# Performance work log

Measured on AMD Instinct MI355X. Metric: run time of the kernel, lower is better.

Reference implementation:

```python
import jax, jax.numpy as jnp
import numpy as np

N = 20000      # nodes per side
E = 160000     # edges
C = 512        # input_channels
C_OUT = 512    # output_channels
TEMP = float(np.sqrt(C))  # self.temperature = sqrt(input_channels)
NEG_SLOPE = 0.01          # LeakyReLU default


def _xavier(key, shape):
    fan_in, fan_out = shape[1], shape[0]
    std = np.sqrt(2.0 / (fan_in + fan_out))
    return jax.random.normal(key, shape, dtype=jnp.float32) * std


def setup_inputs() -> dict:
    key = jax.random.key(0)
    ks = jax.random.split(key, 10)
    return {
        "node_left": jax.random.normal(ks[0], (N, C), dtype=jnp.float32),
        "segmentation_index_left": jax.random.randint(ks[1], (E,), 0, N),
        "index_left": jax.random.randint(ks[2], (E,), 0, N),
        "node_right": jax.random.normal(ks[3], (N, C), dtype=jnp.float32),
        "segmentation_index_right": jax.random.randint(ks[4], (E,), 0, N),
        "index_right": jax.random.randint(ks[5], (E,), 0, N),
        "Wk": _xavier(ks[6], (C, C)),      # key_projection.weight
        "Wv": _xavier(ks[7], (C, C)),      # value_projection.weight
        "Wo": _xavier(ks[8], (C_OUT, C)),  # out_projection Linear weight
        "bo": jnp.zeros((C_OUT,), dtype=jnp.float32),
    }


def segment_softmax(scores, seg_idx, num_segments, temperature):
    # numerically stable softmax over variable-length segments of edges
    s = scores / temperature
    m = jax.ops.segment_max(s, seg_idx, num_segments=num_segments)
    m = jnp.where(jnp.isneginf(m), 0.0, m)  # guard empty segments
    e = jnp.exp(s - m[seg_idx])
    z = jax.ops.segment_sum(e, seg_idx, num_segments=num_segments)
    return e / z[seg_idx]


def _message(translation, seg_idx, num_segments, neighbor, Wo, bo):
    attn = segment_softmax(translation, seg_idx, num_segments, TEMP)  # [E]
    # dropout is identity at inference
    msg = jax.ops.segment_sum(attn[:, None] * neighbor, seg_idx,
                              num_segments=num_segments)  # [N, C]
    h = msg @ Wo.T + bo
    return jnp.where(h >= 0, h, NEG_SLOPE * h)  # LeakyReLU


def reference(node_left, segmentation_index_left, index_left,
              node_right, segmentation_index_right, index_right,
              Wk, Wv, Wo, bo):
    n_left = node_left.shape[0]
    n_right = node_right.shape[0]
    # key projections gathered to edges
    left_center = (node_left @ Wk.T)[segmentation_index_left]    # [E, C]
    right_center = (node_right @ Wk.T)[segmentation_index_right]  # [E, C]
    # value projections gathered to edges (cross side)
    left_neighbor = (node_right @ Wv.T)[segmentation_index_right]  # [E, C]
    right_neighbor = (node_left @ Wv.T)[segmentation_index_left]   # [E, C]
    translation = jnp.sum(left_center * right_center, axis=1)      # [E]
    msg_left = _message(translation, segmentation_index_left, n_left,
                        left_neighbor, Wo, bo)
    msg_right = _message(translation, segmentation_index_right, n_right,
                         right_neighbor, Wo, bo)
    return (msg_left, msg_right)
```

## Files before the change

kernel.cpp:

```cpp
#include <hip/hip_runtime.h>


#define C_DIM 512
#define TEMP_INV (1.0f / 22.627416997969522f)

using bf16x8 = __attribute__((ext_vector_type(8))) __bf16;
using s16x8  = __attribute__((ext_vector_type(8))) short;
using s16x4  = __attribute__((ext_vector_type(4))) short;
using f32x4  = __attribute__((ext_vector_type(4))) float;

__device__ __forceinline__ float bf2f(short u) {
    union { unsigned u; float f; } t;
    t.u = ((unsigned)(unsigned short)u) << 16;
    return t.f;
}
__device__ __forceinline__ short f2bf(float f) {
    union { float f; unsigned u; } t;
    t.f = f;
    unsigned r = t.u + 0x7FFFu + ((t.u >> 16) & 1u);
    return (short)(r >> 16);
}

__global__ void cvt2_f32_bf16(const float* __restrict__ inA,
                              const float* __restrict__ inB,
                              short* __restrict__ out, long n4half) {
    long i = (long)blockIdx.x * blockDim.x + threadIdx.x;
    long stride = (long)gridDim.x * blockDim.x;
    long n4 = 2 * n4half;
    for (; i < n4; i += stride) {
        const float4* src = (i < n4half)
            ? reinterpret_cast<const float4*>(inA) + i
            : reinterpret_cast<const float4*>(inB) + (i - n4half);
        float4 v = *src;
        s16x4 o;
        o[0] = f2bf(v.x); o[1] = f2bf(v.y); o[2] = f2bf(v.z); o[3] = f2bf(v.w);
        reinterpret_cast<s16x4*>(out)[i] = o;
    }
}

__global__ void cvt_weights(const float* __restrict__ Wk,
                            const float* __restrict__ Wv,
                            const float* __restrict__ Wo,
                            short* __restrict__ WkT, short* __restrict__ WvT,
                            short* __restrict__ WoB) {
    int b = blockIdx.x;
    int tid = threadIdx.x;
    if (b < 128) {
        const float* src = (b < 64) ? Wv : Wk;
        short* dst = (b < 64) ? WvT : WkT;
        int bb = b & 63;
        __shared__ float t[64][65];
        int bx = bb & 7, by = bb >> 3;
#pragma unroll
        for (int i = 0; i < 4; ++i) {
            int idx = i * 256 + tid;
            int row = idx >> 4, c4 = idx & 15;
            float4 v = *(const float4*)&src[(size_t)(by * 64 + row) * 512 + bx * 64 + c4 * 4];
            t[row][c4 * 4 + 0] = v.x; t[row][c4 * 4 + 1] = v.y;
            t[row][c4 * 4 + 2] = v.z; t[row][c4 * 4 + 3] = v.w;
        }
        __syncthreads();
#pragma unroll
        for (int i = 0; i < 4; ++i) {
            int idx = i * 256 + tid;
            int row = idx >> 4, g = idx & 15;
            s16x4 o;
            o[0] = f2bf(t[g * 4 + 0][row]);
            o[1] = f2bf(t[g * 4 + 1][row]);
            o[2] = f2bf(t[g * 4 + 2][row]);
            o[3] = f2bf(t[g * 4 + 3][row]);
            *(s16x4*)&dst[(size_t)(bx * 64 + row) * 512 + by * 64 + g * 4] = o;
        }
    } else {
        long base = (long)(b & 63) * 1024;
#pragma unroll
        for (int i = 0; i < 4; ++i) {
            long idx = base + i * 256 + tid;
            float4 v = reinterpret_cast<const float4*>(Wo)[idx];
            s16x4 o;
            o[0] = f2bf(v.x); o[1] = f2bf(v.y); o[2] = f2bf(v.z); o[3] = f2bf(v.w);
            reinterpret_cast<s16x4*>(WoB)[idx] = o;
        }
    }
}

__global__ __launch_bounds__(256, 4)
void gemm_dual(const short* __restrict__ A0, const short* __restrict__ B0,
               short* __restrict__ C0, int M0, int t0,
               const short* __restrict__ A1, const short* __restrict__ B1,
               short* __restrict__ C1, int M1, int total) {
    __shared__ short As[2][128 * 32];
    __shared__ short Bs[2][128 * 32];

    const int bid = blockIdx.x;
    const int q = total >> 3, r = total & 7;
    const int xcd = bid & 7, idx = bid >> 3;
    const int swz = (xcd < r ? xcd * (q + 1) : r * (q + 1) + (xcd - r) * q) + idx;

    const short* A; const short* B; short* Cp; int M; int tile;
    if (swz < t0) { A = A0; B = B0; Cp = C0; M = M0; tile = swz; }
    else          { A = A1; B = B1; Cp = C1; M = M1; tile = swz - t0; }
    const int bm = (tile >> 2) * 128;
    const int bn = (tile & 3) * 128;
    const int K = C_DIM;

    const int tid  = threadIdx.x;
    const int lane = tid & 63;
    const int wid  = tid >> 6;
    const int wm   = (wid >> 1) * 64;
    const int wn   = (wid & 1) * 64;
    const int lrow  = lane & 15;
    const int khalf = lane >> 4;

    auto stage = [&](short* dA, short* dB, int k0) {
#pragma unroll
        for (int j = 0; j < 2; ++j) {
            int L    = j * 256 + tid;
            int pr   = L >> 3;
            int slot = L & 7;
            int g    = slot ^ (pr & 7);
            int row  = pr * 2 + (g >> 2);
            int kg   = g & 3;
            int wb   = (j * 256 + (tid & ~63)) * 16;
            {
                int grow = bm + row; if (grow >= M) grow = M - 1;
                const short* src = A + (size_t)grow * K + k0 + kg * 8;
                __builtin_amdgcn_global_load_lds(
                    (__attribute__((address_space(1))) void*)src,
                    (__attribute__((address_space(3))) void*)((char*)dA + wb),
                    16, 0, 0);
            }
            {
                int grow = bn + row;
                const short* src = B + (size_t)grow * K + k0 + kg * 8;
                __builtin_amdgcn_global_load_lds(
                    (__attribute__((address_space(1))) void*)src,
                    (__attribute__((address_space(3))) void*)((char*)dB + wb),
                    16, 0, 0);
            }
        }
    };

    auto frag = [&](const short* h, int row) -> bf16x8 {
        int pr   = row >> 1;
        int g    = ((row & 1) << 2) | khalf;
        int slot = g ^ (pr & 7);
        return *(const bf16x8*)&h[pr * 64 + slot * 8];
    };

    f32x4 acc[4][4] = {};
    const int nt = K >> 5;

    stage(As[0], Bs[0], 0);

    for (int t = 0; t < nt; ++t) {
        const int cur = t & 1;
        if (t + 1 < nt) {
            stage(As[cur ^ 1], Bs[cur ^ 1], (t + 1) << 5);
            asm volatile("s_waitcnt vmcnt(4)" ::: "memory");
        } else {
            asm volatile("s_waitcnt vmcnt(0)" ::: "memory");
        }
        __builtin_amdgcn_s_barrier();

        const short* as = As[cur];
        const short* bs = Bs[cur];
        bf16x8 af[4], bfr[4];
#pragma unroll
        for (int m = 0; m < 4; ++m) af[m] = frag(as, wm + m * 16 + lrow);
#pragma unroll
        for (int n = 0; n < 4; ++n) bfr[n] = frag(bs, wn + n * 16 + lrow);

        asm volatile("s_waitcnt lgkmcnt(0)" ::: "memory");
        __builtin_amdgcn_sched_barrier(0);
        __builtin_amdgcn_s_barrier();

        __builtin_amdgcn_s_setprio(1);
#pragma unroll
        for (int m = 0; m < 4; ++m)
#pragma unroll
            for (int n = 0; n < 4; ++n)
                acc[m][n] = __builtin_amdgcn_mfma_f32_16x16x32_bf16(
                    af[m], bfr[n], acc[m][n], 0, 0, 0);
        __builtin_amdgcn_s_setprio(0);
    }

    const int crow0 = (lane >> 4) * 4;
    const int ccol  = lane & 15;
#pragma unroll
    for (int m = 0; m < 4; ++m) {
#pragma unroll
        for (int n = 0; n < 4; ++n) {
            int col = bn + wn + n * 16 + ccol;
#pragma unroll
            for (int r2 = 0; r2 < 4; ++r2) {
                int row = bm + wm + m * 16 + crow0 + r2;
                if (row < M) Cp[(size_t)row * C_DIM + col] = f2bf(acc[m][n][r2]);
            }
        }
    }
}

__global__ void count_edges2(const int* __restrict__ segL, const int* __restrict__ segR,
                             int* __restrict__ cnt, int E, int N) {
    int i = blockIdx.x * blockDim.x + threadIdx.x;
    int st = gridDim.x * blockDim.x;
    for (; i < E; i += st) {
        atomicAdd(&cnt[segL[i]], 1);
        atomicAdd(&cnt[N + segR[i]], 1);
    }
}

__global__ void scan_blocks(const int* __restrict__ cnt, int* __restrict__ off,
                            int* __restrict__ bsum, int n) {
    __shared__ int ws[4];
    int tid = threadIdx.x, lane = tid & 63, wid = tid >> 6;
    int i = blockIdx.x * 256 + tid;
    int x = (i < n) ? cnt[i] : 0;
    int v = x;
#pragma unroll
    for (int d = 1; d < 64; d <<= 1) {
        int t = __shfl_up(v, d, 64);
        if (lane >= d) v += t;
    }
    if (lane == 63) ws[wid] = v;
    __syncthreads();
    int woff = 0;
    for (int w = 0; w < wid; ++w) woff += ws[w];
    v += woff;
    if (i < n) off[i + 1] = v;
    if (tid == 255) bsum[blockIdx.x] = v;
}

__global__ void scan_tops(int* __restrict__ bsum, int nb) {
    __shared__ int ws[4];
    int tid = threadIdx.x, lane = tid & 63, wid = tid >> 6;
    int x = (tid < nb) ? bsum[tid] : 0;
    int v = x;
#pragma unroll
    for (int d = 1; d < 64; d <<= 1) {
        int t = __shfl_up(v, d, 64);
        if (lane >= d) v += t;
    }
    if (lane == 63) ws[wid] = v;
    __syncthreads();
    int woff = 0;
    for (int w = 0; w < wid; ++w) woff += ws[w];
    v += woff;
    if (tid < nb) bsum[tid] = v - x;
}

__global__ void scan_apply(int* __restrict__ off, const int* __restrict__ bsum,
                           int* __restrict__ cnt, int n) {
    int i = blockIdx.x * 256 + threadIdx.x;
    if (i < n) {
        off[i + 1] += bsum[blockIdx.x];
        cnt[i] = 0;
    }
    if (i == 0) off[0] = 0;
}

__global__ void edge_dot_fill(const short* __restrict__ KL,
                              const short* __restrict__ KR,
                              const int* __restrict__ segL, const int* __restrict__ segR,
                              const int* __restrict__ off, int* __restrict__ cur,
                              float2* __restrict__ pairs, int E, int N) {
    int e0 = blockIdx.x * 16 + (threadIdx.x >> 6) * 4;
    if (e0 >= E) return;
    int lane = threadIdx.x & 63;

    float sum[4];
#pragma unroll
    for (int k = 0; k < 4; ++k) {
        int ek = e0 + k; if (ek >= E) ek = e0;
        const short* a = KL + (size_t)segL[ek] * 512 + lane * 8;
        const short* b = KR + (size_t)segR[ek] * 512 + lane * 8;
        s16x8 va = *(const s16x8*)a;
        s16x8 vb = *(const s16x8*)b;
        float s = 0.f;
#pragma unroll
        for (int j = 0; j < 8; ++j) s += bf2f(va[j]) * bf2f(vb[j]);
        sum[k] = s;
    }
#pragma unroll
    for (int o = 32; o > 0; o >>= 1) {
#pragma unroll
        for (int k = 0; k < 4; ++k) sum[k] += __shfl_xor(sum[k], o, 64);
    }
    if (lane < 4) {
        int ek = e0 + lane;
        if (ek < E) {
            float s = (lane == 0) ? sum[0] : (lane == 1) ? sum[1]
                    : (lane == 2) ? sum[2] : sum[3];
            float we = __expf(s * TEMP_INV);
            int sl = segL[ek], sr = segR[ek];
            int pl = off[sl] + atomicAdd(&cur[sl], 1);
            pairs[pl] = make_float2(we, __int_as_float(N + sr));
            int pr = off[N + sr] + atomicAdd(&cur[N + sr], 1);
            pairs[pr] = make_float2(we, __int_as_float(sl));
        }
    }
}

__global__ void node_msg(const int* __restrict__ off,
                         const float2* __restrict__ pairs,
                         const short* __restrict__ VW,
                         const float* __restrict__ bo,
                         float* __restrict__ out, int NN2) {
    int n = blockIdx.x * 4 + (threadIdx.x >> 6);
    if (n >= NN2) return;
    int lane = threadIdx.x & 63;
    int beg = off[n], end = off[n + 1];
    const short* VWp = VW + lane * 8;

    float acc[8] = {};
    float z = 0.f;
    int i = beg;
    for (; i + 3 < end; i += 4) {
        float2 p0 = pairs[i], p1 = pairs[i + 1];
        float2 p2 = pairs[i + 2], p3 = pairs[i + 3];
        const s16x8 v0 = *(const s16x8*)(VWp + (size_t)__float_as_int(p0.y) * 512);
        const s16x8 v1 = *(const s16x8*)(VWp + (size_t)__float_as_int(p1.y) * 512);
        const s16x8 v2 = *(const s16x8*)(VWp + (size_t)__float_as_int(p2.y) * 512);
        const s16x8 v3 = *(const s16x8*)(VWp + (size_t)__float_as_int(p3.y) * 512);
        z += (p0.x + p1.x) + (p2.x + p3.x);
#pragma unroll
        for (int j = 0; j < 8; ++j) {
            acc[j] += p0.x * bf2f(v0[j]) + p1.x * bf2f(v1[j]);
            acc[j] += p2.x * bf2f(v2[j]) + p3.x * bf2f(v3[j]);
        }
    }
    for (; i < end; ++i) {
        float2 p = pairs[i];
        const s16x8 v = *(const s16x8*)(VWp + (size_t)__float_as_int(p.y) * 512);
        z += p.x;
#pragma unroll
        for (int j = 0; j < 8; ++j) acc[j] += p.x * bf2f(v[j]);
    }
    float inv = (z > 0.f) ? 1.f / z : 0.f;

    float4 bs0 = *(const float4*)&bo[lane * 8];
    float4 bs1 = *(const float4*)&bo[lane * 8 + 4];
    float bb[8] = {bs0.x, bs0.y, bs0.z, bs0.w, bs1.x, bs1.y, bs1.z, bs1.w};
    f32x4 h0, h1;
#pragma unroll
    for (int j = 0; j < 4; ++j) {
        float v = acc[j] * inv + bb[j];
        h0[j] = v >= 0.f ? v : 0.01f * v;
    }
#pragma unroll
    for (int j = 0; j < 4; ++j) {
        float v = acc[4 + j] * inv + bb[4 + j];
        h1[j] = v >= 0.f ? v : 0.01f * v;
    }
    float* orow = out + (size_t)n * C_DIM + lane * 8;
    __builtin_nontemporal_store(h0, (f32x4*)&orow[0]);
    __builtin_nontemporal_store(h1, (f32x4*)&orow[4]);
}

extern "C" void kernel_launch(void* const* d_in, const int* in_sizes, int n_in,
                              void* d_out, int out_size, void* d_ws, size_t ws_size,
                              hipStream_t stream) {
    const float* node_left  = (const float*)d_in[0];
    const int*   segL       = (const int*)d_in[1];
    const float* node_right = (const float*)d_in[3];
    const int*   segR       = (const int*)d_in[4];
    const float* Wk         = (const float*)d_in[6];
    const float* Wv         = (const float*)d_in[7];
    const float* Wo         = (const float*)d_in[8];
    const float* bo         = (const float*)d_in[9];

    const int C = C_DIM;
    const int N = in_sizes[0] / C;
    const int E = in_sizes[1];
    const int NN2 = 2 * N;

    size_t offb = 0;
    auto alloc = [&](size_t bytes) -> void* {
        void* p = (char*)d_ws + offb;
        offb += (bytes + 255) & ~(size_t)255;
        return p;
    };
    short* nodeLR_b = (short*)alloc((size_t)NN2 * C * 2);
    short* nodeL_b  = nodeLR_b;
    short* nodeR_b  = nodeLR_b + (size_t)N * C;
    short* WkT_b = (short*)alloc((size_t)C * C * 2);
    short* WvT_b = (short*)alloc((size_t)C * C * 2);
    short* Wo_b  = (short*)alloc((size_t)C * C * 2);
    short* Wc_b  = (short*)alloc((size_t)C * C * 2);
    short* G_b   = (short*)alloc((size_t)C * C * 2);
    short* VW    = (short*)alloc((size_t)NN2 * C * 2);
    short* KR2   = (short*)alloc((size_t)N * C * 2);
    float2* pairs = (float2*)alloc((size_t)2 * E * 8);
    int* cnt  = (int*)alloc((size_t)NN2 * 4);
    int* off  = (int*)alloc((size_t)(NN2 + 1) * 4);
    int* bsum = (int*)alloc(256 * 4);

    const int nsb = (NN2 + 255) / 256;

    hipMemsetAsync(cnt, 0, (size_t)NN2 * 4, stream);
    count_edges2<<<512, 256, 0, stream>>>(segL, segR, cnt, E, N);
    scan_blocks<<<nsb, 256, 0, stream>>>(cnt, off, bsum, NN2);
    scan_tops<<<1, 256, 0, stream>>>(bsum, nsb);
    scan_apply<<<nsb, 256, 0, stream>>>(off, bsum, cnt, NN2);

    cvt2_f32_bf16<<<2048, 256, 0, stream>>>(node_left, node_right, nodeLR_b,
                                            (long)N * C / 4);
    cvt_weights<<<192, 256, 0, stream>>>(Wk, Wv, Wo, WkT_b, WvT_b, Wo_b);

    gemm_dual<<<32, 256, 0, stream>>>(Wo_b, WvT_b, Wc_b, C, 16,
                                      WkT_b, WkT_b, G_b, C, 32);

    {
        int t0 = ((NN2 + 127) / 128) * 4;
        int total = t0 + ((N + 127) / 128) * 4;
        gemm_dual<<<total, 256, 0, stream>>>(nodeLR_b, Wc_b, VW, NN2, t0,
                                             nodeR_b, G_b, KR2, N, total);
    }

    edge_dot_fill<<<(E + 15) / 16, 256, 0, stream>>>(nodeL_b, KR2, segL, segR,
                                                     off, cnt, pairs, E, N);

    node_msg<<<(NN2 + 3) / 4, 256, 0, stream>>>(off, pairs, VW, bo,
                                                (float*)d_out, NN2);
}
```

Measured before the change: 211.6 us.

## Bucket edges by left node so each wave reuses its left key row

A new pass first builds a CSR list of right endpoints grouped by left node, using the existing offsets. The edge-score kernel then runs one wave per left node, loads that node's key row once, and computes dot products against the gathered right key rows. Left-side pairs are written contiguously without atomics, which removes the left row gather and half the atomics in the edge pass. The cost is an extra kernel with atomics and a scattered write of the list, plus load imbalance across waves from uneven node degrees.

```diff
diff --git a/kernel.cpp b/kernel.cpp
--- a/kernel.cpp
+++ b/kernel.cpp
@@ -260,44 +260,70 @@
     if (i == 0) off[0] = 0;
 }
 
-__global__ void edge_dot_fill(const short* __restrict__ KL,
-                              const short* __restrict__ KR,
-                              const int* __restrict__ segL, const int* __restrict__ segR,
-                              const int* __restrict__ off, int* __restrict__ cur,
-                              float2* __restrict__ pairs, int E, int N) {
-    int e0 = blockIdx.x * 16 + (threadIdx.x >> 6) * 4;
-    if (e0 >= E) return;
+__global__ void fill_lstL(const int* __restrict__ segL, const int* __restrict__ segR,
+                          const int* __restrict__ off, int* __restrict__ curL,
+                          int* __restrict__ lstL, int E) {
+    int i = blockIdx.x * blockDim.x + threadIdx.x;
+    int st = gridDim.x * blockDim.x;
+    for (; i < E; i += st) {
+        int sl = segL[i];
+        int p = off[sl] + atomicAdd(&curL[sl], 1);
+        lstL[p] = segR[i];
+    }
+}
+
+__global__ void edge_left(const short* __restrict__ nodeL,
+                          const short* __restrict__ KR2,
+                          const int* __restrict__ lstL,
+                          const int* __restrict__ off, int* __restrict__ curR,
+                          float2* __restrict__ pairs, int N) {
+    int n = blockIdx.x * 4 + (threadIdx.x >> 6);
+    if (n >= N) return;
     int lane = threadIdx.x & 63;
-
-    float sum[4];
-#pragma unroll
-    for (int k = 0; k < 4; ++k) {
-        int ek = e0 + k; if (ek >= E) ek = e0;
-        const short* a = KL + (size_t)segL[ek] * 512 + lane * 8;
-        const short* b = KR + (size_t)segR[ek] * 512 + lane * 8;
-        s16x8 va = *(const s16x8*)a;
-        s16x8 vb = *(const s16x8*)b;
-        float s = 0.f;
-#pragma unroll
-        for (int j = 0; j < 8; ++j) s += bf2f(va[j]) * bf2f(vb[j]);
-        sum[k] = s;
-    }
-#pragma unroll
-    for (int o = 32; o > 0; o >>= 1) {
-#pragma unroll
-        for (int k = 0; k < 4; ++k) sum[k] += __shfl_xor(sum[k], o, 64);
-    }
-    if (lane < 4) {
-        int ek = e0 + lane;
-        if (ek < E) {
-            float s = (lane == 0) ? sum[0] : (lane == 1) ? sum[1]
-                    : (lane == 2) ? sum[2] : sum[3];
-            float we = __expf(s * TEMP_INV);
-            int sl = segL[ek], sr = segR[ek];
-            int pl = off[sl] + atomicAdd(&cur[sl], 1);
-            pairs[pl] = make_float2(we, __int_as_float(N + sr));
-            int pr = off[N + sr] + atomicAdd(&cur[N + sr], 1);
-            pairs[pr] = make_float2(we, __int_as_float(sl));
+    int beg = off[n], end = off[n + 1];
+    if (beg == end) return;
+
+    s16x8 kl = *(const s16x8*)(nodeL + (size_t)n * 512 + lane * 8);
+    float klf[8];
+#pragma unroll
+    for (int j = 0; j < 8; ++j) klf[j] = bf2f(kl[j]);
+
+    for (int k0 = beg; k0 < end; k0 += 4) {
+        int sr0, sr1, sr2, sr3;
+        float sum[4];
+        {
+            int k = k0;                       sr0 = lstL[k];
+            k = (k0 + 1 < end) ? k0 + 1 : k0; sr1 = lstL[k];
+            k = (k0 + 2 < end) ? k0 + 2 : k0; sr2 = lstL[k];
+            k = (k0 + 3 < end) ? k0 + 3 : k0; sr3 = lstL[k];
+        }
+        const s16x8 kr0 = *(const s16x8*)(KR2 + (size_t)sr0 * 512 + lane * 8);
+        const s16x8 kr1 = *(const s16x8*)(KR2 + (size_t)sr1 * 512 + lane * 8);
+        const s16x8 kr2 = *(const s16x8*)(KR2 + (size_t)sr2 * 512 + lane * 8);
+        const s16x8 kr3 = *(const s16x8*)(KR2 + (size_t)sr3 * 512 + lane * 8);
+        float s0 = 0.f, s1 = 0.f, s2 = 0.f, s3 = 0.f;
+#pragma unroll
+        for (int j = 0; j < 8; ++j) {
+            s0 += klf[j] * bf2f(kr0[j]);
+            s1 += klf[j] * bf2f(kr1[j]);
+            s2 += klf[j] * bf2f(kr2[j]);
+            s3 += klf[j] * bf2f(kr3[j]);
+        }
+        sum[0] = s0; sum[1] = s1; sum[2] = s2; sum[3] = s3;
+#pragma unroll
+        for (int o = 32; o > 0; o >>= 1)
+#pragma unroll
+            for (int t = 0; t < 4; ++t) sum[t] += __shfl_xor(sum[t], o, 64);
+
+        if (lane < 4 && k0 + lane < end) {
+            float s  = (lane == 0) ? sum[0] : (lane == 1) ? sum[1]
+                     : (lane == 2) ? sum[2] : sum[3];
+            int  srx = (lane == 0) ? sr0 : (lane == 1) ? sr1
+                     : (lane == 2) ? sr2 : sr3;
+            float w = __expf(s * TEMP_INV);
+            pairs[k0 + lane] = make_float2(w, __int_as_float(N + srx));
+            int pr = off[N + srx] + atomicAdd(&curR[N + srx], 1);
+            pairs[pr] = make_float2(w, __int_as_float(n));
         }
     }
 }
@@ -392,6 +418,7 @@
     short* VW    = (short*)alloc((size_t)NN2 * C * 2);
     short* KR2   = (short*)alloc((size_t)N * C * 2);
     float2* pairs = (float2*)alloc((size_t)2 * E * 8);
+    int* lstL = (int*)alloc((size_t)E * 4);
     int* cnt  = (int*)alloc((size_t)NN2 * 4);
     int* off  = (int*)alloc((size_t)(NN2 + 1) * 4);
     int* bsum = (int*)alloc(256 * 4);
@@ -403,6 +430,7 @@
     scan_blocks<<<nsb, 256, 0, stream>>>(cnt, off, bsum, NN2);
     scan_tops<<<1, 256, 0, stream>>>(bsum, nsb);
     scan_apply<<<nsb, 256, 0, stream>>>(off, bsum, cnt, NN2);
+    fill_lstL<<<512, 256, 0, stream>>>(segL, segR, off, cnt, lstL, E);
 
     cvt2_f32_bf16<<<2048, 256, 0, stream>>>(node_left, node_right, nodeLR_b,
                                             (long)N * C / 4);
@@ -418,8 +446,8 @@
                                              nodeR_b, G_b, KR2, N, total);
     }
 
-    edge_dot_fill<<<(E + 15) / 16, 256, 0, stream>>>(nodeL_b, KR2, segL, segR,
-                                                     off, cnt, pairs, E, N);
+    edge_left<<<(N + 3) / 4, 256, 0, stream>>>(nodeL_b, KR2, lstL, off, cnt,
+                                               pairs, N);
 
     node_msg<<<(NN2 + 3) / 4, 256, 0, stream>>>(off, pairs, VW, bo,
                                                 (float*)d_out, NN2);
```

Measured after the change: 201.3 us. 1.05x faster.
